# Optimization experiments

Hardware: AMD Instinct MI355X
Metric: run time of the kernel (lower is better)

## Reference

```python
import math
import jax, jax.numpy as jnp
import numpy as np

NP_, NA_ = 100000, 50000
IN_DIM = OUT_DIM = 128
H, DK = 4, 32
E_CITES, E_WRITES, E_REV = 600000, 300000, 300000


def setup_inputs() -> dict:
    key = jax.random.key(0)
    ks = jax.random.split(key, 16)
    s_in = 1.0 / math.sqrt(IN_DIM)   # ~ Linear default init scale
    s_dk = 1.0 / math.sqrt(DK)       # ~ xavier for d_k x d_k
    return {
        "h_paper": jax.random.normal(ks[0], (NP_, IN_DIM), jnp.float32),
        "h_author": jax.random.normal(ks[1], (NA_, IN_DIM), jnp.float32),
        "Wk": jax.random.normal(ks[2], (2, OUT_DIM, IN_DIM), jnp.float32) * s_in,
        "bk": jnp.zeros((2, OUT_DIM), jnp.float32),
        "Wq": jax.random.normal(ks[3], (2, OUT_DIM, IN_DIM), jnp.float32) * s_in,
        "bq": jnp.zeros((2, OUT_DIM), jnp.float32),
        "Wv": jax.random.normal(ks[4], (2, OUT_DIM, IN_DIM), jnp.float32) * s_in,
        "bv": jnp.zeros((2, OUT_DIM), jnp.float32),
        "Wa": jax.random.normal(ks[5], (2, OUT_DIM, OUT_DIM), jnp.float32) * s_in,
        "ba": jnp.zeros((2, OUT_DIM), jnp.float32),
        "rel_att": jax.random.normal(ks[6], (3, H, DK, DK), jnp.float32) * s_dk,
        "rel_msg": jax.random.normal(ks[7], (3, H, DK, DK), jnp.float32) * s_dk,
        "rel_pri": jnp.ones((3, H), jnp.float32),
        "skip": jnp.ones((2,), jnp.float32),
        "cites_src": jax.random.randint(ks[8], (E_CITES,), 0, NP_, jnp.int32),
        "cites_dst": jax.random.randint(ks[9], (E_CITES,), 0, NP_, jnp.int32),
        "writes_src": jax.random.randint(ks[10], (E_WRITES,), 0, NA_, jnp.int32),
        "writes_dst": jax.random.randint(ks[11], (E_WRITES,), 0, NP_, jnp.int32),
        "rev_src": jax.random.randint(ks[12], (E_REV,), 0, NP_, jnp.int32),
        "rev_dst": jax.random.randint(ks[13], (E_REV,), 0, NA_, jnp.int32),
    }


def _seg_softmax(scores, seg, n):
    # edge softmax normalized by destination node (DGL edge_softmax, norm_by='dst')
    m = jax.ops.segment_max(scores, seg, num_segments=n)
    e = jnp.exp(scores - m[seg])
    z = jax.ops.segment_sum(e, seg, num_segments=n)
    return e / z[seg]


def reference(h_paper, h_author, Wk, bk, Wq, bq, Wv, bv, Wa, ba,
              rel_att, rel_msg, rel_pri, skip,
              cites_src, cites_dst, writes_src, writes_dst, rev_src, rev_dst):
    sqrt_dk = math.sqrt(DK)

    def proj(h, W, b, t):
        return (h @ W[t].T + b[t]).reshape(-1, H, DK)  # [N, H, dk]

    def rel_agg(h_src, h_dst, ts, td, e, src, dst, n_dst):
        # relation-specific transforms of k and v (per-head dk x dk matmul)
        k = jnp.einsum('nhi,hij->nhj', proj(h_src, Wk, bk, ts), rel_att[e])
        v = jnp.einsum('nhi,hij->nhj', proj(h_src, Wv, bv, ts), rel_msg[e])
        q = proj(h_dst, Wq, bq, td)
        # per-edge attention logits: (q_dst . k_src) * pri / sqrt(dk)  -> [E, H]
        score = jnp.einsum('ehd,ehd->eh', q[dst], k[src]) * rel_pri[e] / sqrt_dk
        a = _seg_softmax(score, dst, n_dst)
        # weighted scatter-sum of messages to destination nodes
        return jax.ops.segment_sum(v[src] * a[:, :, None], dst, num_segments=n_dst)

    # cross_reducer='mean': average per-relation aggregates per dst node type
    t_paper = (rel_agg(h_paper, h_paper, 0, 0, 0, cites_src, cites_dst, NP_) +
               rel_agg(h_author, h_paper, 1, 0, 1, writes_src, writes_dst, NP_)) * 0.5
    t_author = rel_agg(h_paper, h_author, 0, 1, 2, rev_src, rev_dst, NA_)

    def out(t, h, nt):
        trans = t.reshape(-1, OUT_DIM) @ Wa[nt].T + ba[nt]  # dropout = identity (eval)
        alpha = jax.nn.sigmoid(skip[nt])
        return trans * alpha + h * (1.0 - alpha)

    return jnp.concatenate([out(t_paper, h_paper, 0), out(t_author, h_author, 1)], axis=0)
```

## Files before the change

kernel.cpp:

```cpp
#include <hip/hip_runtime.h>
#include <hip/hip_bf16.h>
#include <math.h>

#define NP 100000
#define NA 50000
#define DIM 128
#define NH 4
#define DKK 32
#define EC 600000
#define EW 300000
#define ER 300000
#define CAP 32

#define CDIV(a,b) (((a)+(b)-1)/(b))

typedef __attribute__((ext_vector_type(8))) short bf16x8;
typedef __attribute__((ext_vector_type(4))) float f32x4;

__device__ __forceinline__ ushort f2b(float f){
  unsigned u = __float_as_uint(f);
  unsigned r = u + 0x7FFFu + ((u>>16)&1u);
  return (ushort)(r>>16);
}
__device__ __forceinline__ float blo(unsigned u){ return __uint_as_float(u<<16); }
__device__ __forceinline__ float bhi(unsigned u){ return __uint_as_float(u & 0xFFFF0000u); }

struct C2Args { const float4* in[2]; uint2* out[2]; };
__global__ void k_cast2(C2Args a){
  int s = blockIdx.y;
  int i = blockIdx.x*256 + threadIdx.x;
  float4 v = a.in[s][i];
  uint2 o;
  o.x = (unsigned)f2b(v.x) | ((unsigned)f2b(v.y)<<16);
  o.y = (unsigned)f2b(v.z) | ((unsigned)f2b(v.w)<<16);
  a.out[s][i] = o;
}

__global__ void k_zero_i(int* p, int n){
  int i = blockIdx.x*blockDim.x + threadIdx.x;
  if (i < n) p[i] = 0;
}

__global__ void k_fuse(const float* __restrict__ Wk, const float* __restrict__ bk,
                       const float* __restrict__ Wv, const float* __restrict__ bv,
                       const float* __restrict__ rel_att, const float* __restrict__ rel_msg,
                       ushort* __restrict__ Wfb_all, float* __restrict__ bfu_all){
  int rel = blockIdx.x >> 7;
  int ts = (rel==1) ? 1 : 0;
  ushort* Wfb = Wfb_all + rel*32768;
  float*  bfu = bfu_all + rel*256;
  int idx = (blockIdx.x & 127)*256 + threadIdx.x;
  int which = idx >> 14;
  int rem = idx & 16383;
  int op = rem >> 7;
  int j  = rem & 127;
  int h = op >> 5, jp = op & 31;
  const float* W  = which ? Wv : Wk;
  const float* R  = which ? rel_msg : rel_att;
  const float* Wt = W + (size_t)ts*DIM*DIM;
  const float* Re = R + (((size_t)rel*NH + h)*DKK)*DKK + jp;
  float acc = 0.f;
  #pragma unroll
  for (int i=0;i<DKK;i++) acc += Wt[(h*DKK+i)*DIM + j] * Re[(size_t)i*DKK];
  Wfb[which*16384 + op*DIM + j] = f2b(acc);
  if (idx < 256){
    int w2 = idx >> 7; int op2 = idx & 127; int h2 = op2>>5, jp2 = op2&31;
    const float* bsrc = (w2 ? bv : bk) + (size_t)ts*DIM;
    const float* R2 = (w2 ? rel_msg : rel_att) + (((size_t)rel*NH + h2)*DKK)*DKK + jp2;
    float accb = 0.f;
    #pragma unroll
    for (int i=0;i<DKK;i++) accb += bsrc[h2*DKK+i]*R2[(size_t)i*DKK];
    bfu[w2*DIM + op2] = accb;
  }
}

struct MArgs {
  const float* X[3];
  const ushort* W[3][3];
  const float* b[3][3];
  ushort* Y[3][3];
  int N[3];
  int npan[3];
  int base[3];
};
__global__ __launch_bounds__(512) void k_mega(MArgs g){
  int b = blockIdx.x;
  int seg = (b >= g.base[2]) ? 2 : ((b >= g.base[1]) ? 1 : 0);
  int local = b - g.base[seg];
  int N = g.N[seg];
  int tile = local*64;
  if (tile >= N) return;
  int tid = threadIdx.x;
  int wv = tid >> 6, l = tid & 63;
  int lr = l & 15, lk = l >> 4;
  int rowg = wv >> 1, colg = wv & 1;
  int arow = tile + rowg*16 + lr;
  int ar = (arow < N) ? arow : 0;
  const float4* Ar = (const float4*)(g.X[seg] + (size_t)ar*DIM);
  bf16x8 A[4];
  #pragma unroll
  for (int kc=0;kc<4;kc++){
    float4 u = Ar[kc*8 + lk*2];
    float4 v = Ar[kc*8 + lk*2 + 1];
    bf16x8 a;
    a[0]=(short)f2b(u.x); a[1]=(short)f2b(u.y); a[2]=(short)f2b(u.z); a[3]=(short)f2b(u.w);
    a[4]=(short)f2b(v.x); a[5]=(short)f2b(v.y); a[6]=(short)f2b(v.z); a[7]=(short)f2b(v.w);
    A[kc] = a;
  }
  __shared__ __align__(16) ushort Wl[128*136];
  __shared__ __align__(16) ushort Ost[64*136];
  uint4* Wl4 = (uint4*)Wl;
  int npan = g.npan[seg];
  for (int p=0; p<npan; ++p){
    const uint4* Ws = (const uint4*)g.W[seg][p];
    #pragma unroll
    for (int i=0;i<4;i++){
      int idx = i*512 + tid;
      uint4 v = Ws[idx];
      int r = idx >> 4, c = idx & 15;
      Wl4[r*17 + c] = v;
    }
    __syncthreads();
    const float* bias = g.b[seg][p];
    #pragma unroll
    for (int ct=0; ct<4; ct++){
      int col = colg*64 + ct*16 + lr;
      f32x4 acc = {0.f,0.f,0.f,0.f};
      #pragma unroll
      for (int kc=0;kc<4;kc++){
        bf16x8 B = *(const bf16x8*)&Wl[col*136 + kc*32 + lk*8];
        acc = __builtin_amdgcn_mfma_f32_16x16x32_bf16(A[kc], B, acc, 0, 0, 0);
      }
      float bv = bias[col];
      #pragma unroll
      for (int j=0;j<4;j++)
        Ost[(rowg*16 + lk*4 + j)*136 + col] = f2b(acc[j] + bv);
    }
    __syncthreads();
    int orow = tid >> 3;
    int oseg = (tid & 7)*2;
    int grow = tile + orow;
    if (grow < N){
      uint4* dst = (uint4*)(g.Y[seg][p] + (size_t)grow*DIM);
      const uint4* s = (const uint4*)Ost;
      dst[oseg]   = s[orow*17 + oseg];
      dst[oseg+1] = s[orow*17 + oseg + 1];
    }
    __syncthreads();
  }
}

struct BArgs { const int* dst[3]; const int* src[3]; int* cnt[3]; int* slots[3]; int E[3]; int n[3]; };
__global__ void k_bucket(BArgs a){
  int r = blockIdx.y;
  int E = a.E[r], n = a.n[r];
  const int* dst = a.dst[r];
  const int* srcv = a.src[r];
  int* cnt = a.cnt[r];
  int* slots = a.slots[r];
  int g = blockIdx.x & 7;
  int sub = blockIdx.x >> 3;
  int chunk = (n + 7) >> 3;
  int lo = g*chunk;
  int hi = lo + chunk; if (hi > n) hi = n;
  int per = (E + 255) >> 8;
  per = (per + 3) & ~3;
  int e0 = sub*per;
  int e1 = e0 + per; if (e1 > E) e1 = E;
  for (int i = e0 + threadIdx.x*4; i < e1; i += 256*4){
    if (i + 4 <= e1){
      int4 d = *(const int4*)(dst + i);
      int4 s = *(const int4*)(srcv + i);
      if (d.x>=lo && d.x<hi){ int p=atomicAdd(&cnt[d.x],1); if(p<CAP) slots[(size_t)d.x*CAP+p]=s.x; }
      if (d.y>=lo && d.y<hi){ int p=atomicAdd(&cnt[d.y],1); if(p<CAP) slots[(size_t)d.y*CAP+p]=s.y; }
      if (d.z>=lo && d.z<hi){ int p=atomicAdd(&cnt[d.z],1); if(p<CAP) slots[(size_t)d.z*CAP+p]=s.z; }
      if (d.w>=lo && d.w<hi){ int p=atomicAdd(&cnt[d.w],1); if(p<CAP) slots[(size_t)d.w*CAP+p]=s.w; }
    } else {
      for (int j=i; j<e1; ++j){
        int d = dst[j];
        if (d>=lo && d<hi){ int p=atomicAdd(&cnt[d],1); if(p<CAP) slots[(size_t)d*CAP+p]=srcv[j]; }
      }
    }
  }
}

__device__ __forceinline__ void agg_bucket(const unsigned* __restrict__ K2,
    const unsigned* __restrict__ V2, const int* __restrict__ slots,
    int deg, int nsrc, float qx, float qy, float prih, int lane,
    float& o0, float& o1)
{
  const int4* sl4 = (const int4*)slots;
  float m = -INFINITY, z = 0.f, a0 = 0.f, a1 = 0.f;
  for (int i = 0; i < deg; i += 4){
    int4 s4 = sl4[i>>2];
    int s0 = ((unsigned)s4.x < (unsigned)nsrc) ? s4.x : 0;
    int s1 = ((unsigned)s4.y < (unsigned)nsrc) ? s4.y : 0;
    int s2 = ((unsigned)s4.z < (unsigned)nsrc) ? s4.z : 0;
    int s3 = ((unsigned)s4.w < (unsigned)nsrc) ? s4.w : 0;
    bool v1 = (i+1 < deg), v2 = (i+2 < deg), v3 = (i+3 < deg);
    unsigned ku0 = K2[(size_t)s0*64 + lane];
    unsigned ku1 = K2[(size_t)s1*64 + lane];
    unsigned ku2 = K2[(size_t)s2*64 + lane];
    unsigned ku3 = K2[(size_t)s3*64 + lane];
    unsigned vu0 = V2[(size_t)s0*64 + lane];
    unsigned vu1 = V2[(size_t)s1*64 + lane];
    unsigned vu2 = V2[(size_t)s2*64 + lane];
    unsigned vu3 = V2[(size_t)s3*64 + lane];
    float p0 = qx*blo(ku0) + qy*bhi(ku0);
    float p1 = qx*blo(ku1) + qy*bhi(ku1);
    float p2 = qx*blo(ku2) + qy*bhi(ku2);
    float p3 = qx*blo(ku3) + qy*bhi(ku3);
    #pragma unroll
    for (int d=1; d<16; d<<=1){
      p0 += __shfl_xor(p0, d);
      p1 += __shfl_xor(p1, d);
      p2 += __shfl_xor(p2, d);
      p3 += __shfl_xor(p3, d);
    }
    float sc0 = p0*prih;
    float sc1 = v1 ? p1*prih : -INFINITY;
    float sc2 = v2 ? p2*prih : -INFINITY;
    float sc3 = v3 ? p3*prih : -INFINITY;
    float mx = fmaxf(fmaxf(sc0,sc1), fmaxf(sc2,sc3));
    float nm = fmaxf(m, mx);
    float wo = __expf(m - nm);
    float e0 = __expf(sc0-nm), e1 = __expf(sc1-nm), e2 = __expf(sc2-nm), e3 = __expf(sc3-nm);
    z  = z*wo + ((e0+e1)+(e2+e3));
    a0 = a0*wo + (e0*blo(vu0) + e1*blo(vu1) + e2*blo(vu2) + e3*blo(vu3));
    a1 = a1*wo + (e0*bhi(vu0) + e1*bhi(vu1) + e2*bhi(vu2) + e3*bhi(vu3));
    m = nm;
  }
  float inv = (z > 0.f)? 1.f/z : 0.f;
  o0 = a0*inv; o1 = a1*inv;
}

__global__ __launch_bounds__(256) void k_attnP(const unsigned* __restrict__ Q2,
    const unsigned* __restrict__ K0, const unsigned* __restrict__ V0,
    const unsigned* __restrict__ K1, const unsigned* __restrict__ V1,
    const int* __restrict__ slots0, const int* __restrict__ cnt0,
    const int* __restrict__ slots1, const int* __restrict__ cnt1,
    const float* __restrict__ pri, float* __restrict__ t)
{
  int w = blockIdx.x*4 + (threadIdx.x>>6);
  if (w >= NP) return;
  int lane = threadIdx.x & 63;
  int h = lane >> 4;
  unsigned qu = Q2[(size_t)w*64 + lane];
  float qx = blo(qu), qy = bhi(qu);
  float pri0 = pri[h]      * 0.17677669529663687f;
  float pri1 = pri[NH + h] * 0.17677669529663687f;
  int d0 = cnt0[w]; if (d0 > CAP) d0 = CAP;
  int d1 = cnt1[w]; if (d1 > CAP) d1 = CAP;
  float x0, x1, y0, y1;
  agg_bucket(K0, V0, slots0 + (size_t)w*CAP, d0, NP, qx, qy, pri0, lane, x0, x1);
  agg_bucket(K1, V1, slots1 + (size_t)w*CAP, d1, NA, qx, qy, pri1, lane, y0, y1);
  float2* tb = (float2*)(t + (size_t)w*DIM);
  float2 o = {x0 + y0, x1 + y1};
  tb[lane] = o;
}

__global__ __launch_bounds__(256) void k_attn1(const unsigned* __restrict__ Q2,
    const unsigned* __restrict__ K2, const unsigned* __restrict__ V2,
    const int* __restrict__ slots, const int* __restrict__ cnt,
    const float* __restrict__ pri, int ndst, int nsrc, float* __restrict__ t)
{
  int w = blockIdx.x*4 + (threadIdx.x>>6);
  if (w >= ndst) return;
  int lane = threadIdx.x & 63;
  int h = lane >> 4;
  unsigned qu = Q2[(size_t)w*64 + lane];
  float qx = blo(qu), qy = bhi(qu);
  float prih = pri[h] * 0.17677669529663687f;
  int deg = cnt[w]; if (deg > CAP) deg = CAP;
  float o0, o1;
  agg_bucket(K2, V2, slots + (size_t)w*CAP, deg, nsrc, qx, qy, prih, lane, o0, o1);
  float2* tb = (float2*)(t + (size_t)w*DIM);
  float2 o = {o0, o1};
  tb[lane] = o;
}

struct FArgs { const float* X[2]; const ushort* W[2]; const float* b[2]; const float* h[2];
               float* out[2]; float scale[2]; int N[2]; const float* skip; };
__global__ __launch_bounds__(256) void k_fingemm(FArgs g){
  int y = blockIdx.y;
  int N = g.N[y];
  if ((int)blockIdx.x*32 >= N) return;
  const float* X = g.X[y];
  const ushort* Wb = g.W[y];
  const float* bias = g.b[y];
  const float* hin = g.h[y];
  float* out = g.out[y];
  float scale = g.scale[y];
  int tid = threadIdx.x;
  int wv = tid >> 6;
  int l  = tid & 63;
  int lr = l & 15, lk = l >> 4;
  int r0 = blockIdx.x*32 + (wv&1)*16;
  int c0 = (wv>>1)*64;
  int arow = r0 + lr;
  int ar = (arow < N) ? arow : 0;
  const float4* Ar = (const float4*)(X + (size_t)ar*DIM);
  bf16x8 A[4];
  #pragma unroll
  for (int kc=0;kc<4;kc++){
    float4 u = Ar[kc*8 + lk*2];
    float4 v = Ar[kc*8 + lk*2 + 1];
    bf16x8 a;
    a[0]=(short)f2b(u.x); a[1]=(short)f2b(u.y); a[2]=(short)f2b(u.z); a[3]=(short)f2b(u.w);
    a[4]=(short)f2b(v.x); a[5]=(short)f2b(v.y); a[6]=(short)f2b(v.z); a[7]=(short)f2b(v.w);
    A[kc] = a;
  }
  __shared__ float Ls[32][132];
  #pragma unroll
  for (int ct=0; ct<4; ct++){
    int col = c0 + ct*16 + lr;
    const bf16x8* Wrow = (const bf16x8*)(Wb + (size_t)col*DIM);
    f32x4 acc = {0.f,0.f,0.f,0.f};
    #pragma unroll
    for (int kc=0;kc<4;kc++)
      acc = __builtin_amdgcn_mfma_f32_16x16x32_bf16(A[kc], Wrow[kc*4+lk], acc, 0, 0, 0);
    float bv = bias[col];
    #pragma unroll
    for (int j=0;j<4;j++){
      int lrow = (wv&1)*16 + lk*4 + j;
      Ls[lrow][col] = scale*acc[j] + bv;
    }
  }
  __syncthreads();
  float alpha = 1.f/(1.f + expf(-g.skip[y]));
  float beta  = 1.f - alpha;
  int orow = tid >> 3;
  int ocb  = (tid & 7)*16;
  int row  = blockIdx.x*32 + orow;
  if (row < N){
    const float4* H4 = (const float4*)hin;
    float4* O4 = (float4*)out;
    #pragma unroll
    for (int q=0;q<4;q++){
      float4 tv = *(const float4*)&Ls[orow][ocb + q*4];
      float4 hv = H4[(size_t)row*32 + (ocb>>2) + q];
      float4 o;
      o.x = alpha*tv.x + beta*hv.x;
      o.y = alpha*tv.y + beta*hv.y;
      o.z = alpha*tv.z + beta*hv.z;
      o.w = alpha*tv.w + beta*hv.w;
      O4[(size_t)row*32 + (ocb>>2) + q] = o;
    }
  }
}

extern "C" void kernel_launch(void* const* d_in, const int* in_sizes, int n_in,
                              void* d_out, int out_size, void* d_ws, size_t ws_size,
                              hipStream_t stream) {
  const float* h_paper = (const float*)d_in[0];
  const float* h_author= (const float*)d_in[1];
  const float* Wk = (const float*)d_in[2];
  const float* bk = (const float*)d_in[3];
  const float* Wq = (const float*)d_in[4];
  const float* bq = (const float*)d_in[5];
  const float* Wv = (const float*)d_in[6];
  const float* bv = (const float*)d_in[7];
  const float* Wa = (const float*)d_in[8];
  const float* ba = (const float*)d_in[9];
  const float* rel_att = (const float*)d_in[10];
  const float* rel_msg = (const float*)d_in[11];
  const float* rel_pri = (const float*)d_in[12];
  const float* skip    = (const float*)d_in[13];
  const int* cites_src = (const int*)d_in[14];
  const int* cites_dst = (const int*)d_in[15];
  const int* writes_src= (const int*)d_in[16];
  const int* writes_dst= (const int*)d_in[17];
  const int* rev_src   = (const int*)d_in[18];
  const int* rev_dst   = (const int*)d_in[19];

  ushort* qbP = (ushort*)d_ws;
  ushort* qbA = qbP + (size_t)NP*DIM;
  ushort* K0  = qbA + (size_t)NA*DIM;
  ushort* V0  = K0  + (size_t)NP*DIM;
  ushort* K1  = V0  + (size_t)NP*DIM;
  ushort* V1  = K1  + (size_t)NA*DIM;
  ushort* K2  = V1  + (size_t)NA*DIM;
  ushort* V2  = K2  + (size_t)NP*DIM;
  ushort* Wqb = V2  + (size_t)NP*DIM;
  ushort* Wab = Wqb + 32768;
  ushort* Wfb = Wab + 32768;
  float*  bfu = (float*)(Wfb + 3*32768);
  int* ib = (int*)(bfu + 3*256);
  const int NDST_TOT = 2*NP + NA;
  int* cnt_all   = ib;           ib += NDST_TOT;
  int* slots_all = ib;

  float* t_paper  = (float*)d_out;
  float* t_author = (float*)d_out + (size_t)NP*DIM;

  const int cntB[3] = {0, NP, 2*NP};

  {
    C2Args a;
    a.in[0]=(const float4*)Wq; a.out[0]=(uint2*)Wqb;
    a.in[1]=(const float4*)Wa; a.out[1]=(uint2*)Wab;
    k_cast2<<<dim3(32,2),256,0,stream>>>(a);
  }
  k_fuse<<<384,256,0,stream>>>(Wk, bk, Wv, bv, rel_att, rel_msg, Wfb, bfu);
  k_zero_i<<<CDIV(NDST_TOT,256),256,0,stream>>>(cnt_all, NDST_TOT);
  {
    BArgs b;
    const int* dsts[3] = {cites_dst, writes_dst, rev_dst};
    const int* srcs[3] = {cites_src, writes_src, rev_src};
    int Es[3] = {EC, EW, ER};
    int ns[3] = {NP, NP, NA};
    for (int r=0;r<3;r++){
      b.dst[r]=dsts[r]; b.src[r]=srcs[r];
      b.cnt[r]=cnt_all+cntB[r];
      b.slots[r]=slots_all+(size_t)cntB[r]*CAP;
      b.E[r]=Es[r]; b.n[r]=ns[r];
    }
    k_bucket<<<dim3(2048,3),256,0,stream>>>(b);
  }
  {
    const int T0 = CDIV(NP,64), T1 = CDIV(NA,64), T2 = CDIV(NP,64);
    MArgs m;
    m.base[0]=0; m.base[1]=T0; m.base[2]=T0+T1;
    m.X[0]=h_paper;  m.N[0]=NP; m.npan[0]=3;
    m.W[0][0]=Wqb;        m.b[0][0]=bq;        m.Y[0][0]=qbP;
    m.W[0][1]=Wfb;        m.b[0][1]=bfu;       m.Y[0][1]=K0;
    m.W[0][2]=Wfb+16384;  m.b[0][2]=bfu+DIM;   m.Y[0][2]=V0;
    m.X[1]=h_author; m.N[1]=NA; m.npan[1]=3;
    m.W[1][0]=Wqb+16384;        m.b[1][0]=bq+DIM;        m.Y[1][0]=qbA;
    m.W[1][1]=Wfb+32768;        m.b[1][1]=bfu+256;       m.Y[1][1]=K1;
    m.W[1][2]=Wfb+32768+16384;  m.b[1][2]=bfu+256+DIM;   m.Y[1][2]=V1;
    m.X[2]=h_paper;  m.N[2]=NP; m.npan[2]=3;
    m.npan[2]=2;
    m.W[2][0]=Wfb+2*32768;        m.b[2][0]=bfu+512;       m.Y[2][0]=K2;
    m.W[2][1]=Wfb+2*32768+16384;  m.b[2][1]=bfu+512+DIM;   m.Y[2][1]=V2;
    m.W[2][2]=Wfb;                m.b[2][2]=bfu;           m.Y[2][2]=K2;
    k_mega<<<T0+T1+T2,512,0,stream>>>(m);
  }
  k_attnP<<<CDIV(NP,4),256,0,stream>>>((const unsigned*)qbP,
      (const unsigned*)K0, (const unsigned*)V0,
      (const unsigned*)K1, (const unsigned*)V1,
      slots_all+(size_t)cntB[0]*CAP, cnt_all+cntB[0],
      slots_all+(size_t)cntB[1]*CAP, cnt_all+cntB[1],
      rel_pri, t_paper);
  k_attn1<<<CDIV(NA,4),256,0,stream>>>((const unsigned*)qbA,
      (const unsigned*)K2, (const unsigned*)V2,
      slots_all+(size_t)cntB[2]*CAP, cnt_all+cntB[2], rel_pri+2*NH, NA, NP, t_author);
  {
    FArgs f;
    f.X[0]=t_paper;   f.W[0]=Wab;        f.b[0]=ba;     f.h[0]=h_paper;
    f.out[0]=t_paper;  f.scale[0]=0.5f; f.N[0]=NP;
    f.X[1]=t_author;  f.W[1]=Wab+16384;  f.b[1]=ba+DIM; f.h[1]=h_author;
    f.out[1]=t_author; f.scale[1]=1.0f; f.N[1]=NA;
    f.skip = skip;
    k_fingemm<<<dim3(CDIV(NP,32),2),256,0,stream>>>(f);
  }
}
```

Baseline: 360.6 us.

## Compute attention scores edge-per-lane and merge paper/author attention kernels

The edge-attention aggregation is restructured so that each lane of a 16-lane head group owns one edge. It loads that edge's full 32-wide K slice with vector loads and computes the dot product locally, which replaces the per-edge cross-lane shuffle reductions. Softmax max and sum now use one shuffle reduction per chunk of 16 edges. V accumulation broadcasts the source index and weight via shuffles. The two attention kernels are also merged into a single launch covering paper and author destinations, relying on the slot and count buffers being laid out contiguously as NP, NP, NA. In exchange, K loads become gathered 64-byte rows per lane and register use rises from holding 32 q floats.

```diff
diff --git a/kernel.cpp b/kernel.cpp
--- a/kernel.cpp
+++ b/kernel.cpp
@@ -11,6 +11,7 @@
 #define EW 300000
 #define ER 300000
 #define CAP 32
+#define SCL 0.17677669529663687f
 
 #define CDIV(a,b) (((a)+(b)-1)/(b))
 
@@ -184,99 +185,110 @@
   }
 }
 
-__device__ __forceinline__ void agg_bucket(const unsigned* __restrict__ K2,
+__device__ __forceinline__ void agg16(const ushort* __restrict__ Kb,
     const unsigned* __restrict__ V2, const int* __restrict__ slots,
-    int deg, int nsrc, float qx, float qy, float prih, int lane,
+    int deg, int nsrc, const float* qf, float prih, int lane,
     float& o0, float& o1)
 {
-  const int4* sl4 = (const int4*)slots;
+  int e = lane & 15;
+  int hb = (lane >> 4) * 32;
   float m = -INFINITY, z = 0.f, a0 = 0.f, a1 = 0.f;
-  for (int i = 0; i < deg; i += 4){
-    int4 s4 = sl4[i>>2];
-    int s0 = ((unsigned)s4.x < (unsigned)nsrc) ? s4.x : 0;
-    int s1 = ((unsigned)s4.y < (unsigned)nsrc) ? s4.y : 0;
-    int s2 = ((unsigned)s4.z < (unsigned)nsrc) ? s4.z : 0;
-    int s3 = ((unsigned)s4.w < (unsigned)nsrc) ? s4.w : 0;
-    bool v1 = (i+1 < deg), v2 = (i+2 < deg), v3 = (i+3 < deg);
-    unsigned ku0 = K2[(size_t)s0*64 + lane];
-    unsigned ku1 = K2[(size_t)s1*64 + lane];
-    unsigned ku2 = K2[(size_t)s2*64 + lane];
-    unsigned ku3 = K2[(size_t)s3*64 + lane];
-    unsigned vu0 = V2[(size_t)s0*64 + lane];
-    unsigned vu1 = V2[(size_t)s1*64 + lane];
-    unsigned vu2 = V2[(size_t)s2*64 + lane];
-    unsigned vu3 = V2[(size_t)s3*64 + lane];
-    float p0 = qx*blo(ku0) + qy*bhi(ku0);
-    float p1 = qx*blo(ku1) + qy*bhi(ku1);
-    float p2 = qx*blo(ku2) + qy*bhi(ku2);
-    float p3 = qx*blo(ku3) + qy*bhi(ku3);
-    #pragma unroll
-    for (int d=1; d<16; d<<=1){
-      p0 += __shfl_xor(p0, d);
-      p1 += __shfl_xor(p1, d);
-      p2 += __shfl_xor(p2, d);
-      p3 += __shfl_xor(p3, d);
-    }
-    float sc0 = p0*prih;
-    float sc1 = v1 ? p1*prih : -INFINITY;
-    float sc2 = v2 ? p2*prih : -INFINITY;
-    float sc3 = v3 ? p3*prih : -INFINITY;
-    float mx = fmaxf(fmaxf(sc0,sc1), fmaxf(sc2,sc3));
+  for (int c = 0; c < deg; c += 16){
+    int ecnt = deg - c; if (ecnt > 16) ecnt = 16;
+    bool act = (e < ecnt);
+    int sl = 0;
+    if (act){ int s = slots[c + e]; sl = ((unsigned)s < (unsigned)nsrc) ? s : 0; }
+    const uint4* kr = (const uint4*)(Kb + (size_t)sl*DIM + hb);
+    unsigned ku[16];
+    *(uint4*)&ku[0]  = kr[0];
+    *(uint4*)&ku[4]  = kr[1];
+    *(uint4*)&ku[8]  = kr[2];
+    *(uint4*)&ku[12] = kr[3];
+    float d = 0.f;
+    #pragma unroll
+    for (int i=0;i<16;i++) d = fmaf(qf[2*i], blo(ku[i]), fmaf(qf[2*i+1], bhi(ku[i]), d));
+    float sc = act ? d * prih : -INFINITY;
+    float mx = sc;
+    mx = fmaxf(mx, __shfl_xor(mx, 1));
+    mx = fmaxf(mx, __shfl_xor(mx, 2));
+    mx = fmaxf(mx, __shfl_xor(mx, 4));
+    mx = fmaxf(mx, __shfl_xor(mx, 8));
     float nm = fmaxf(m, mx);
     float wo = __expf(m - nm);
-    float e0 = __expf(sc0-nm), e1 = __expf(sc1-nm), e2 = __expf(sc2-nm), e3 = __expf(sc3-nm);
-    z  = z*wo + ((e0+e1)+(e2+e3));
-    a0 = a0*wo + (e0*blo(vu0) + e1*blo(vu1) + e2*blo(vu2) + e3*blo(vu3));
-    a1 = a1*wo + (e0*bhi(vu0) + e1*bhi(vu1) + e2*bhi(vu2) + e3*bhi(vu3));
+    float a  = __expf(sc - nm);
+    float zs = a;
+    zs += __shfl_xor(zs, 1);
+    zs += __shfl_xor(zs, 2);
+    zs += __shfl_xor(zs, 4);
+    zs += __shfl_xor(zs, 8);
+    z = z*wo + zs;
+    a0 *= wo; a1 *= wo;
+    int ab = lane & 48;
+    for (int j = 0; j < ecnt; j += 4){
+      int s0 = __shfl(sl, j+0);
+      int s1 = __shfl(sl, j+1);
+      int s2 = __shfl(sl, j+2);
+      int s3 = __shfl(sl, j+3);
+      float aj0 = __shfl(a, ab + j+0);
+      float aj1 = __shfl(a, ab + j+1);
+      float aj2 = __shfl(a, ab + j+2);
+      float aj3 = __shfl(a, ab + j+3);
+      unsigned vu0 = V2[(size_t)s0*64 + lane];
+      unsigned vu1 = V2[(size_t)s1*64 + lane];
+      unsigned vu2 = V2[(size_t)s2*64 + lane];
+      unsigned vu3 = V2[(size_t)s3*64 + lane];
+      a0 += aj0*blo(vu0) + aj1*blo(vu1) + aj2*blo(vu2) + aj3*blo(vu3);
+      a1 += aj0*bhi(vu0) + aj1*bhi(vu1) + aj2*bhi(vu2) + aj3*bhi(vu3);
+    }
     m = nm;
   }
-  float inv = (z > 0.f)? 1.f/z : 0.f;
+  float inv = (z > 0.f) ? 1.f/z : 0.f;
   o0 = a0*inv; o1 = a1*inv;
 }
 
-__global__ __launch_bounds__(256) void k_attnP(const unsigned* __restrict__ Q2,
-    const unsigned* __restrict__ K0, const unsigned* __restrict__ V0,
-    const unsigned* __restrict__ K1, const unsigned* __restrict__ V1,
-    const int* __restrict__ slots0, const int* __restrict__ cnt0,
-    const int* __restrict__ slots1, const int* __restrict__ cnt1,
-    const float* __restrict__ pri, float* __restrict__ t)
+__global__ __launch_bounds__(256) void k_attnM(
+    const ushort* __restrict__ qbP, const ushort* __restrict__ qbA,
+    const ushort* __restrict__ K0, const unsigned* __restrict__ V0,
+    const ushort* __restrict__ K1, const unsigned* __restrict__ V1,
+    const ushort* __restrict__ K2, const unsigned* __restrict__ V2,
+    const int* __restrict__ slots_all, const int* __restrict__ cnt_all,
+    const float* __restrict__ pri, float* __restrict__ t_paper, float* __restrict__ t_author)
 {
   int w = blockIdx.x*4 + (threadIdx.x>>6);
-  if (w >= NP) return;
+  if (w >= NP+NA) return;
   int lane = threadIdx.x & 63;
   int h = lane >> 4;
-  unsigned qu = Q2[(size_t)w*64 + lane];
-  float qx = blo(qu), qy = bhi(qu);
-  float pri0 = pri[h]      * 0.17677669529663687f;
-  float pri1 = pri[NH + h] * 0.17677669529663687f;
-  int d0 = cnt0[w]; if (d0 > CAP) d0 = CAP;
-  int d1 = cnt1[w]; if (d1 > CAP) d1 = CAP;
-  float x0, x1, y0, y1;
-  agg_bucket(K0, V0, slots0 + (size_t)w*CAP, d0, NP, qx, qy, pri0, lane, x0, x1);
-  agg_bucket(K1, V1, slots1 + (size_t)w*CAP, d1, NA, qx, qy, pri1, lane, y0, y1);
-  float2* tb = (float2*)(t + (size_t)w*DIM);
-  float2 o = {x0 + y0, x1 + y1};
-  tb[lane] = o;
-}
-
-__global__ __launch_bounds__(256) void k_attn1(const unsigned* __restrict__ Q2,
-    const unsigned* __restrict__ K2, const unsigned* __restrict__ V2,
-    const int* __restrict__ slots, const int* __restrict__ cnt,
-    const float* __restrict__ pri, int ndst, int nsrc, float* __restrict__ t)
-{
-  int w = blockIdx.x*4 + (threadIdx.x>>6);
-  if (w >= ndst) return;
-  int lane = threadIdx.x & 63;
-  int h = lane >> 4;
-  unsigned qu = Q2[(size_t)w*64 + lane];
-  float qx = blo(qu), qy = bhi(qu);
-  float prih = pri[h] * 0.17677669529663687f;
-  int deg = cnt[w]; if (deg > CAP) deg = CAP;
-  float o0, o1;
-  agg_bucket(K2, V2, slots + (size_t)w*CAP, deg, nsrc, qx, qy, prih, lane, o0, o1);
-  float2* tb = (float2*)(t + (size_t)w*DIM);
-  float2 o = {o0, o1};
-  tb[lane] = o;
+  bool isP = (w < NP);
+  int wn = isP ? w : w - NP;
+  const ushort* qb = isP ? qbP : qbA;
+  float qf[32];
+  {
+    const uint4* qr = (const uint4*)(qb + (size_t)wn*DIM + h*32);
+    unsigned qu[16];
+    *(uint4*)&qu[0]  = qr[0];
+    *(uint4*)&qu[4]  = qr[1];
+    *(uint4*)&qu[8]  = qr[2];
+    *(uint4*)&qu[12] = qr[3];
+    #pragma unroll
+    for (int i=0;i<16;i++){ qf[2*i] = blo(qu[i]); qf[2*i+1] = bhi(qu[i]); }
+  }
+  if (isP){
+    int d0 = cnt_all[wn];      if (d0 > CAP) d0 = CAP;
+    int d1 = cnt_all[NP + wn]; if (d1 > CAP) d1 = CAP;
+    float x0,x1,y0,y1;
+    agg16(K0, V0, slots_all + (size_t)wn*CAP,        d0, NP, qf, pri[h]*SCL,      lane, x0, x1);
+    agg16(K1, V1, slots_all + ((size_t)NP+wn)*CAP,   d1, NA, qf, pri[NH+h]*SCL,   lane, y0, y1);
+    float2* tb = (float2*)(t_paper + (size_t)wn*DIM);
+    float2 o = {x0 + y0, x1 + y1};
+    tb[lane] = o;
+  } else {
+    int d2 = cnt_all[2*NP + wn]; if (d2 > CAP) d2 = CAP;
+    float r0, r1;
+    agg16(K2, V2, slots_all + ((size_t)2*NP+wn)*CAP, d2, NP, qf, pri[2*NH+h]*SCL, lane, r0, r1);
+    float2* tb = (float2*)(t_author + (size_t)wn*DIM);
+    float2 o = {r0, r1};
+    tb[lane] = o;
+  }
 }
 
 struct FArgs { const float* X[2]; const ushort* W[2]; const float* b[2]; const float* h[2];
@@ -429,22 +441,15 @@
     m.W[1][0]=Wqb+16384;        m.b[1][0]=bq+DIM;        m.Y[1][0]=qbA;
     m.W[1][1]=Wfb+32768;        m.b[1][1]=bfu+256;       m.Y[1][1]=K1;
     m.W[1][2]=Wfb+32768+16384;  m.b[1][2]=bfu+256+DIM;   m.Y[1][2]=V1;
-    m.X[2]=h_paper;  m.N[2]=NP; m.npan[2]=3;
-    m.npan[2]=2;
+    m.X[2]=h_paper;  m.N[2]=NP; m.npan[2]=2;
     m.W[2][0]=Wfb+2*32768;        m.b[2][0]=bfu+512;       m.Y[2][0]=K2;
     m.W[2][1]=Wfb+2*32768+16384;  m.b[2][1]=bfu+512+DIM;   m.Y[2][1]=V2;
     m.W[2][2]=Wfb;                m.b[2][2]=bfu;           m.Y[2][2]=K2;
     k_mega<<<T0+T1+T2,512,0,stream>>>(m);
   }
-  k_attnP<<<CDIV(NP,4),256,0,stream>>>((const unsigned*)qbP,
-      (const unsigned*)K0, (const unsigned*)V0,
-      (const unsigned*)K1, (const unsigned*)V1,
-      slots_all+(size_t)cntB[0]*CAP, cnt_all+cntB[0],
-      slots_all+(size_t)cntB[1]*CAP, cnt_all+cntB[1],
-      rel_pri, t_paper);
-  k_attn1<<<CDIV(NA,4),256,0,stream>>>((const unsigned*)qbA,
-      (const unsigned*)K2, (const unsigned*)V2,
-      slots_all+(size_t)cntB[2]*CAP, cnt_all+cntB[2], rel_pri+2*NH, NA, NP, t_author);
+  k_attnM<<<CDIV(NP+NA,4),256,0,stream>>>(qbP, qbA,
+      K0, (const unsigned*)V0, K1, (const unsigned*)V1, K2, (const unsigned*)V2,
+      slots_all, cnt_all, rel_pri, t_paper, t_author);
   {
     FArgs f;
     f.X[0]=t_paper;   f.W[0]=Wab;        f.b[0]=ba;     f.h[0]=h_paper;
```

Measured after the change: 431.3 us. 19.6% more time.
